# Kernel tuning notes

Hardware: AMD Instinct MI355X
Metric: run time of the kernel (lower is better)

Reference implementation:

```python
import jax, jax.numpy as jnp
import numpy as np

EPS = 1e-5  # torch LayerNorm default

def layernorm(x, gamma, beta):
    mu = jnp.mean(x, axis=-1, keepdims=True)
    var = jnp.mean(jnp.square(x - mu), axis=-1, keepdims=True)
    return (x - mu) * jax.lax.rsqrt(var + EPS) * gamma + beta

def setup_inputs() -> dict:
    key = jax.random.key(0)
    ks = jax.random.split(key, 8)
    B, S, D = 4, 2048, 1024
    s = 1.0 / np.sqrt(D)  # torch Linear init scale
    return {
        "x": jax.random.normal(ks[0], (B, S, D), dtype=jnp.float32),
        "Wq": jax.random.uniform(ks[1], (D, D), jnp.float32, -s, s),
        "bq": jax.random.uniform(ks[2], (D,), jnp.float32, -s, s),
        "Wk": jax.random.uniform(ks[3], (D, D), jnp.float32, -s, s),
        "bk": jax.random.uniform(ks[4], (D,), jnp.float32, -s, s),
        "Wv": jax.random.uniform(ks[5], (D, D), jnp.float32, -s, s),
        "bv": jax.random.uniform(ks[6], (D,), jnp.float32, -s, s),
        "gamma": jnp.ones((D,), jnp.float32),
        "beta": jnp.zeros((D,), jnp.float32),
    }

def reference(x, Wq, bq, Wk, bk, Wv, bv, gamma, beta):
    # torch Linear: x @ W.T + b; shared LayerNorm applied to each projection
    q = layernorm(jnp.einsum('bsd,ed->bse', x, Wq) + bq, gamma, beta)
    k = layernorm(jnp.einsum('bsd,ed->bse', x, Wk) + bk, gamma, beta)
    v = layernorm(jnp.einsum('bsd,ed->bse', x, Wv) + bv, gamma, beta)
    att = jnp.einsum('bqd,bkd->bqk', q, k)  # no 1/sqrt(d) scaling in original
    att = jax.nn.softmax(att, axis=-1)
    # dropout is identity in eval mode (reference baseline)
    return jnp.einsum('bqk,bkd->bqd', att, v)
```

## Files before the change

### kernel.cpp

```cpp
#include <hip/hip_runtime.h>

typedef _Float16 f16;
typedef __attribute__((ext_vector_type(4))) _Float16 f16x4;
typedef __attribute__((ext_vector_type(8))) _Float16 f16x8;
typedef __attribute__((ext_vector_type(4))) float f32x4;

#define GLB_AS __attribute__((address_space(1)))
#define LDS_AS __attribute__((address_space(3)))

__device__ __forceinline__ void async_copy16(const void* g, void* l) {
  __builtin_amdgcn_global_load_lds((const GLB_AS void*)g, (LDS_AS void*)l, 16, 0, 0);
}

template <typename OutT, int MODE, bool BIAS>
__global__ __launch_bounds__(256) void gemm_kn(
    const f16* __restrict__ A, const f16* __restrict__ B, OutT* __restrict__ C,
    int lda, int ldb, int ldc, int K, long sA, long sB, long sC,
    int tiles_x, int tiles_y,
    const float* __restrict__ b0, const float* __restrict__ b1,
    const float* __restrict__ b2)
{
  constexpr int BM = 128, BK = 32;
  __shared__ __align__(16) f16 Ash[BM * BK];
  __shared__ __align__(16) f16 Bsh[BM * BK];

  int bx, by, bz;
  {
    const int n = blockIdx.x;
    if (MODE == 0) {
      by = n % tiles_y;
      const int r = n / tiles_y;
      bx = r % tiles_x;
      bz = r / tiles_x;
    } else {
      const int j = n & 7, i = n >> 3;
      bz = j >> 1;
      bx = i >> 3;
      by = (j & 1) * 8 + (i & 7);
    }
  }

  A += (long)bz * sA;
  B += (long)bz * sB;
  C += (long)bz * sC;

  const int tid  = threadIdx.x;
  const int wave = tid >> 6, lane = tid & 63;
  const int m0 = by * BM, n0 = bx * BM;
  const int wm = (wave >> 1) * 64, wn = (wave & 1) * 64;

  const int srow = wave * 32 + (lane >> 2);
  const int skb  = (lane & 3) * 8;
  const f16* Ag = A + (long)(m0 + srow) * lda + skb;
  const f16* Bg = B + (long)(n0 + srow) * ldb + skb;
  f16* As0 = &Ash[(wave * 32) * BK];
  f16* As1 = &Ash[(wave * 32 + 16) * BK];
  f16* Bs0 = &Bsh[(wave * 32) * BK];
  f16* Bs1 = &Bsh[(wave * 32 + 16) * BK];

  f32x4 acc[4][4] = {};
  const int r16 = lane & 15, quad = lane >> 4;

  for (int k0 = 0; k0 < K; k0 += BK) {
    async_copy16(Ag + k0,                  As0);
    async_copy16(Ag + k0 + 16 * (long)lda, As1);
    async_copy16(Bg + k0,                  Bs0);
    async_copy16(Bg + k0 + 16 * (long)ldb, Bs1);
    __syncthreads();

    f16x8 af[4], bf[4];
#pragma unroll
    for (int i = 0; i < 4; i++) {
      af[i] = *(const f16x8*)&Ash[(wm + i * 16 + r16) * BK + quad * 8];
      bf[i] = *(const f16x8*)&Bsh[(wn + i * 16 + r16) * BK + quad * 8];
    }
#pragma unroll
    for (int i = 0; i < 4; i++)
#pragma unroll
      for (int j = 0; j < 4; j++)
        acc[i][j] = __builtin_amdgcn_mfma_f32_16x16x32_f16(af[i], bf[j], acc[i][j], 0, 0, 0);
    __syncthreads();
  }

  float bias_j[4] = {0.f, 0.f, 0.f, 0.f};
  if (BIAS) {
    const float* bias = (bz == 0) ? b0 : (bz == 1) ? b1 : b2;
#pragma unroll
    for (int j = 0; j < 4; j++) bias_j[j] = bias[n0 + wn + j * 16 + r16];
  }
#pragma unroll
  for (int i = 0; i < 4; i++)
#pragma unroll
    for (int j = 0; j < 4; j++)
#pragma unroll
      for (int r = 0; r < 4; r++) {
        long row = m0 + wm + i * 16 + quad * 4 + r;
        long col = n0 + wn + j * 16 + r16;
        C[row * (long)ldc + col] = (OutT)(acc[i][j][r] + bias_j[j]);
      }
}

__global__ __launch_bounds__(256) void cast_all(
    const float* __restrict__ x, const float* __restrict__ Wq,
    const float* __restrict__ Wk, const float* __restrict__ Wv,
    f16* __restrict__ Xh, f16* __restrict__ Wh)
{
  const long off = (long)blockIdx.x * 1024 + threadIdx.x * 4;
  const float* src;
  f16* dst;
  if (off < 8388608L) {
    src = x + off;
    dst = Xh + off;
  } else {
    const long o = off - 8388608L;
    src = (o < 1048576L) ? Wq + o
        : (o < 2097152L) ? Wk + (o - 1048576L)
                         : Wv + (o - 2097152L);
    dst = Wh + o;
  }
  const float4 v = *(const float4*)src;
  f16x4 h;
  h.x = (f16)v.x; h.y = (f16)v.y; h.z = (f16)v.z; h.w = (f16)v.w;
  *(f16x4*)dst = h;
}

__global__ __launch_bounds__(256) void ln_kernel(
    f16* __restrict__ P, const float* __restrict__ gamma,
    const float* __restrict__ beta)
{
  f16* p = P + (long)blockIdx.y * 8388608 + (long)blockIdx.x * 1024;
  const int tid = threadIdx.x;
  const int e = tid * 4;

  f16x4 raw = *(const f16x4*)(p + e);
  float v0 = (float)raw.x, v1 = (float)raw.y;
  float v2 = (float)raw.z, v3 = (float)raw.w;
  float s  = v0 + v1 + v2 + v3;
  float s2 = v0 * v0 + v1 * v1 + v2 * v2 + v3 * v3;

#pragma unroll
  for (int off = 32; off > 0; off >>= 1) {
    s  += __shfl_down(s, off, 64);
    s2 += __shfl_down(s2, off, 64);
  }
  __shared__ float red[10];
  const int wave = tid >> 6, lane = tid & 63;
  if (lane == 0) { red[wave] = s; red[4 + wave] = s2; }
  __syncthreads();
  if (tid == 0) {
    red[8] = red[0] + red[1] + red[2] + red[3];
    red[9] = red[4] + red[5] + red[6] + red[7];
  }
  __syncthreads();
  const float mu   = red[8] * (1.f / 1024.f);
  const float var  = red[9] * (1.f / 1024.f) - mu * mu;
  const float rstd = rsqrtf(var + 1e-5f);

  float4 gg = *(const float4*)(gamma + e);
  float4 be = *(const float4*)(beta + e);
  f16x4 o;
  o.x = (f16)((v0 - mu) * rstd * gg.x + be.x);
  o.y = (f16)((v1 - mu) * rstd * gg.y + be.y);
  o.z = (f16)((v2 - mu) * rstd * gg.z + be.z);
  o.w = (f16)((v3 - mu) * rstd * gg.w + be.w);
  *(f16x4*)(p + e) = o;
}

__global__ __launch_bounds__(256) void transpose_kernel(const f16* __restrict__ V,
                                                        f16* __restrict__ Vt)
{
  const int S = 2048, D = 1024;
  const f16* v = V + (long)blockIdx.z * ((long)S * D);
  f16* vt = Vt + (long)blockIdx.z * ((long)D * S);
  __shared__ f16 tile[64][66];
  const int d0 = blockIdx.x * 64, j0 = blockIdx.y * 64;
  const int tx = threadIdx.x & 63, ty = threadIdx.x >> 6;
#pragma unroll
  for (int r = ty; r < 64; r += 4)
    tile[r][tx] = v[(long)(j0 + r) * D + d0 + tx];
  __syncthreads();
#pragma unroll
  for (int r = ty; r < 64; r += 4)
    vt[(long)(d0 + r) * S + j0 + tx] = tile[tx][r];
}

__global__ __launch_bounds__(256) void softmax_kernel(float* __restrict__ Sc)
{
  float* srow = Sc + (long)blockIdx.x * 2048;
  const int tid = threadIdx.x;
  float4 a = ((const float4*)srow)[tid];
  float4 b = ((const float4*)srow)[256 + tid];

  float m = fmaxf(fmaxf(fmaxf(a.x, a.y), fmaxf(a.z, a.w)),
                  fmaxf(fmaxf(b.x, b.y), fmaxf(b.z, b.w)));
#pragma unroll
  for (int off = 32; off > 0; off >>= 1) m = fmaxf(m, __shfl_down(m, off, 64));
  __shared__ float red[6];
  const int wave = tid >> 6, lane = tid & 63;
  if (lane == 0) red[wave] = m;
  __syncthreads();
  if (tid == 0) red[4] = fmaxf(fmaxf(red[0], red[1]), fmaxf(red[2], red[3]));
  __syncthreads();
  const float M = red[4];

  a.x = __expf(a.x - M); a.y = __expf(a.y - M);
  a.z = __expf(a.z - M); a.w = __expf(a.w - M);
  b.x = __expf(b.x - M); b.y = __expf(b.y - M);
  b.z = __expf(b.z - M); b.w = __expf(b.w - M);
  float s = a.x + a.y + a.z + a.w + b.x + b.y + b.z + b.w;
#pragma unroll
  for (int off = 32; off > 0; off >>= 1) s += __shfl_down(s, off, 64);
  if (lane == 0) red[wave] = s;
  __syncthreads();
  if (tid == 0) red[5] = red[0] + red[1] + red[2] + red[3];
  __syncthreads();
  const float inv = 1.0f / red[5];

  f16* orow = (f16*)srow;
  f16x4 oa, ob;
  oa.x = (f16)(a.x * inv); oa.y = (f16)(a.y * inv);
  oa.z = (f16)(a.z * inv); oa.w = (f16)(a.w * inv);
  ob.x = (f16)(b.x * inv); ob.y = (f16)(b.y * inv);
  ob.z = (f16)(b.z * inv); ob.w = (f16)(b.w * inv);
  ((f16x4*)orow)[tid]       = oa;
  ((f16x4*)orow)[256 + tid] = ob;
}

extern "C" void kernel_launch(void* const* d_in, const int* in_sizes, int n_in,
                              void* d_out, int out_size, void* d_ws, size_t ws_size,
                              hipStream_t stream)
{
  const float* x     = (const float*)d_in[0];
  const float* Wq    = (const float*)d_in[1];
  const float* bq    = (const float*)d_in[2];
  const float* Wk    = (const float*)d_in[3];
  const float* bk    = (const float*)d_in[4];
  const float* Wv    = (const float*)d_in[5];
  const float* bv    = (const float*)d_in[6];
  const float* gamma = (const float*)d_in[7];
  const float* beta  = (const float*)d_in[8];
  float* out = (float*)d_out;

  char* ws = (char*)d_ws;
  f16*   P  = (f16*)(ws);
  f16*   Vt = (f16*)(ws + (48u << 20));
  float* Sc = (float*)(ws + (64u << 20));
  f16*   Xh = (f16*)(ws + (64u << 20));
  f16*   Wh = (f16*)(ws + (80u << 20));

  cast_all<<<11264, 256, 0, stream>>>(x, Wq, Wk, Wv, Xh, Wh);

  gemm_kn<f16, 0, true><<<1536, 256, 0, stream>>>(
      Xh, Wh, P, 1024, 1024, 1024, 1024, 0L, 1048576L, 8388608L,
      8, 64, bq, bk, bv);

  ln_kernel<<<dim3(8192, 3), 256, 0, stream>>>(P, gamma, beta);

  transpose_kernel<<<dim3(16, 32, 4), 256, 0, stream>>>(P + 2L * 8388608, Vt);

  gemm_kn<float, 1, false><<<1024, 256, 0, stream>>>(
      P, P + 8388608, Sc, 1024, 1024, 2048, 1024, 2097152L, 2097152L, 4194304L,
      16, 16, nullptr, nullptr, nullptr);

  softmax_kernel<<<8192, 256, 0, stream>>>(Sc);

  gemm_kn<float, 1, false><<<512, 256, 0, stream>>>(
      (const f16*)Sc, Vt, out, 4096, 2048, 1024, 2048, 8388608L, 2097152L, 2097152L,
      8, 16, nullptr, nullptr, nullptr);
}
```

Before: 333.2 us.

## Double-buffer LDS tiles in the GEMM kernel to overlap loads with MFMA

Splits the A and B shared-memory tiles into two buffers. The first K-tile is prefetched before the loop, and each iteration issues the async global-to-LDS copy for the next tile before running MFMAs on the current one. This removes one barrier per iteration and is meant to hide global load latency behind compute. The cost is twice the LDS per block, which could reduce occupancy.

```diff
diff --git a/kernel.cpp b/kernel.cpp
--- a/kernel.cpp
+++ b/kernel.cpp
@@ -21,8 +21,8 @@
     const float* __restrict__ b2)
 {
   constexpr int BM = 128, BK = 32;
-  __shared__ __align__(16) f16 Ash[BM * BK];
-  __shared__ __align__(16) f16 Bsh[BM * BK];
+  __shared__ __align__(16) f16 Ash[2][BM * BK];
+  __shared__ __align__(16) f16 Bsh[2][BM * BK];
 
   int bx, by, bz;
   {
@@ -48,38 +48,46 @@
   const int wave = tid >> 6, lane = tid & 63;
   const int m0 = by * BM, n0 = bx * BM;
   const int wm = (wave >> 1) * 64, wn = (wave & 1) * 64;
+  const int r16 = lane & 15, quad = lane >> 4;
 
   const int srow = wave * 32 + (lane >> 2);
   const int skb  = (lane & 3) * 8;
   const f16* Ag = A + (long)(m0 + srow) * lda + skb;
   const f16* Bg = B + (long)(n0 + srow) * ldb + skb;
-  f16* As0 = &Ash[(wave * 32) * BK];
-  f16* As1 = &Ash[(wave * 32 + 16) * BK];
-  f16* Bs0 = &Bsh[(wave * 32) * BK];
-  f16* Bs1 = &Bsh[(wave * 32 + 16) * BK];
+  const int lo0 = (wave * 32) * BK;
+  const int lo1 = (wave * 32 + 16) * BK;
+
+  async_copy16(Ag,                  &Ash[0][lo0]);
+  async_copy16(Ag + 16 * (long)lda, &Ash[0][lo1]);
+  async_copy16(Bg,                  &Bsh[0][lo0]);
+  async_copy16(Bg + 16 * (long)ldb, &Bsh[0][lo1]);
 
   f32x4 acc[4][4] = {};
-  const int r16 = lane & 15, quad = lane >> 4;
-
-  for (int k0 = 0; k0 < K; k0 += BK) {
-    async_copy16(Ag + k0,                  As0);
-    async_copy16(Ag + k0 + 16 * (long)lda, As1);
-    async_copy16(Bg + k0,                  Bs0);
-    async_copy16(Bg + k0 + 16 * (long)ldb, Bs1);
+
+  int buf = 0;
+  for (int k0 = 0; k0 < K; k0 += BK, buf ^= 1) {
     __syncthreads();
 
+    if (k0 + BK < K) {
+      const int nb = buf ^ 1;
+      const long k1 = k0 + BK;
+      async_copy16(Ag + k1,                  &Ash[nb][lo0]);
+      async_copy16(Ag + k1 + 16 * (long)lda, &Ash[nb][lo1]);
+      async_copy16(Bg + k1,                  &Bsh[nb][lo0]);
+      async_copy16(Bg + k1 + 16 * (long)ldb, &Bsh[nb][lo1]);
+    }
+
     f16x8 af[4], bf[4];
 #pragma unroll
     for (int i = 0; i < 4; i++) {
-      af[i] = *(const f16x8*)&Ash[(wm + i * 16 + r16) * BK + quad * 8];
-      bf[i] = *(const f16x8*)&Bsh[(wn + i * 16 + r16) * BK + quad * 8];
+      af[i] = *(const f16x8*)&Ash[buf][(wm + i * 16 + r16) * BK + quad * 8];
+      bf[i] = *(const f16x8*)&Bsh[buf][(wn + i * 16 + r16) * BK + quad * 8];
     }
 #pragma unroll
     for (int i = 0; i < 4; i++)
 #pragma unroll
       for (int j = 0; j < 4; j++)
         acc[i][j] = __builtin_amdgcn_mfma_f32_16x16x32_f16(af[i], bf[j], acc[i][j], 0, 0, 0);
-    __syncthreads();
   }
 
   float bias_j[4] = {0.f, 0.f, 0.f, 0.f};
```

Result: faster. 309.4 us (-7.1%).
